# Optimization experiments

Hardware: AMD Instinct MI355X
Metric: run time of the kernel (lower is better)

## Reference

```python
import jax, jax.numpy as jnp
import numpy as np

V, C, T, H, HS, HID, L = 8000, 256, 256, 4, 64, 1024, 2
B = 2


def _ln(x, g, b, eps=1e-5):
    mu = jnp.mean(x, axis=-1, keepdims=True)
    var = jnp.var(x, axis=-1, keepdims=True)
    return (x - mu) * jax.lax.rsqrt(var + eps) * g + b


def setup_inputs() -> dict:
    key = jax.random.key(0)
    ks = iter(jax.random.split(key, 32))
    n = lambda shape: jax.random.normal(next(ks), shape, dtype=jnp.float32) * 0.02
    inp = {
        "idx": jax.random.randint(next(ks), (B, T), 0, V),
        "tok_emb": n((V, C)),
        # distance positional embedding params
        "pos_table": n((T, C)),
        "pos_w1": n((C, 2 * C)),
        "pos_w2": n((2 * C, 2 * C)),
        "pos_b2": n((2 * C,)),
        "pos_ln_g": jnp.ones((2 * C,), jnp.float32),
        "pos_ln_b": jnp.zeros((2 * C,), jnp.float32),
        # per-layer, per-head attention-MLP params (stacked over L, H)
        "att_w1": n((L, H, 2 * C, C)),
        "att_w2": n((L, H, C)),
        "att_b2": n((L, H)),
        "val_w": n((L, H, C, HS)),
        "proj_w": n((L, C, C)),
        "proj_b": n((L, C)),
        "ln2_g": jnp.ones((L, C), jnp.float32),
        "ln2_b": jnp.zeros((L, C), jnp.float32),
        "ff_w1": n((L, C, HID)),
        "ff_w2": n((L, HID, C)),
        "ff_b2": n((L, C)),
        "lnf_g": jnp.ones((C,), jnp.float32),
        "lnf_b": jnp.zeros((C,), jnp.float32),
        "head_w": n((C, V)),
        "head_b": n((V,)),
    }
    return inp


def reference(idx, tok_emb, pos_table, pos_w1, pos_w2, pos_b2, pos_ln_g, pos_ln_b,
              att_w1, att_w2, att_b2, val_w, proj_w, proj_b, ln2_g, ln2_b,
              ff_w1, ff_w2, ff_b2, lnf_g, lnf_b, head_w, head_b):
    b, t = idx.shape
    gelu = lambda x: jax.nn.gelu(x, approximate=False)

    # distance positional embedding: tril(i - j) indices into table
    ar = jnp.arange(t)
    dist = jnp.tril(ar[:, None] - ar[None, :])            # [t,t] in [0, t)
    pe = pos_table[dist]                                   # [t,t,C]
    pe = gelu(pe @ pos_w1) @ pos_w2 + pos_b2               # [t,t,2C]
    pe = _ln(pe, pos_ln_g, pos_ln_b)                       # [t,t,2C]

    mask = jnp.tril(jnp.ones((t, t), bool))                # causal
    scale = C ** (-0.5)

    x = tok_emb[idx]                                       # [b,t,C]
    for l in range(L):
        # pairwise concat(key, query) + pos emb, shared across heads
        kk = jnp.broadcast_to(x[:, None, :, :], (b, t, t, C))   # k[b,i,j]=x[b,j]
        qq = jnp.broadcast_to(x[:, :, None, :], (b, t, t, C))   # q[b,i,j]=x[b,i]
        a2 = jnp.concatenate([kk, qq], axis=-1) + pe[None]       # [b,t,t,2C]
        h1 = gelu(jnp.einsum('btsz,hzc->bhtsc', a2, att_w1[l]))  # [b,H,t,t,C]
        wei = jnp.einsum('bhtsc,hc->bhts', h1, att_w2[l]) + att_b2[l][None, :, None, None]
        wei = wei * scale
        wei = jnp.where(mask[None, None], wei, -jnp.inf)
        wei = jax.nn.softmax(wei, axis=-1)                       # [b,H,t,t]
        v = jnp.einsum('btc,hcd->bhtd', x, val_w[l])             # [b,H,t,HS]
        out = jnp.einsum('bhts,bhsd->bhtd', wei, v)              # [b,H,t,HS]
        out = out.transpose(0, 2, 1, 3).reshape(b, t, H * HS)    # concat heads
        x = x + out @ proj_w[l] + proj_b[l]
        h = _ln(x, ln2_g[l], ln2_b[l])
        x = x + gelu(h @ ff_w1[l]) @ ff_w2[l] + ff_b2[l]
    x = _ln(x, lnf_g, lnf_b)
    logits = x @ head_w + head_b                                 # [b,t,V]
    return logits
```

## Files before the change

### kernel.cpp

```cpp
#include <hip/hip_runtime.h>
#include <hip/hip_bf16.h>
#include <math.h>

constexpr int TDIM = 256;
constexpr int CDIM = 256;
constexpr int NH   = 4;
constexpr int DHS  = 64;
constexpr int FHID = 1024;
constexpr int NV   = 8000;
constexpr int NB   = 2;

typedef __attribute__((ext_vector_type(8))) short bf16x8;
typedef __attribute__((ext_vector_type(4))) float f32x4;
typedef __attribute__((ext_vector_type(2))) float f32x2;
typedef __attribute__((ext_vector_type(4))) unsigned int uint4v;

__device__ __forceinline__ float gelu_f(float x) {
    return 0.5f * x * (1.0f + erff(x * 0.70710678118654752440f));
}

__device__ __forceinline__ f32x2 gelu2p(f32x2 x) {
    constexpr float A = 0.7814073f, B = -0.1075621f, C = 0.00904825f, D = -0.000293447f;
    f32x2 xc;
    xc.x = fminf(fmaxf(x.x, -3.4f), 3.4f);
    xc.y = fminf(fmaxf(x.y, -3.4f), 3.4f);
    f32x2 u = xc * xc;
    f32x2 h = u * D + C;
    h = h * u + B;
    h = h * u + A;
    f32x2 g = xc * h;
    f32x2 t = x * 0.5f;
    return t * g + t;
}

__device__ __forceinline__ unsigned short f2bf(float f) {
    unsigned int u = __float_as_uint(f);
    unsigned int r = (u + 0x7FFF + ((u >> 16) & 1)) >> 16;
    return (unsigned short)r;
}

__global__ __launch_bounds__(256) void k_tcast_all(
    const float* __restrict__ head_w, const float* __restrict__ att_w1,
    const float* __restrict__ ff_w1, const float* __restrict__ ff_w2,
    const float* __restrict__ val_w, const float* __restrict__ proj_w,
    unsigned short* __restrict__ wT, unsigned short* __restrict__ W1r,
    unsigned short* __restrict__ Wff1, unsigned short* __restrict__ Wff2,
    unsigned short* __restrict__ Wv, unsigned short* __restrict__ Wproj)
{
    int q = blockIdx.x;
    const float* src; unsigned short* dst; int R, C, tx, ty;
    if (q < 2000)      { src = head_w; dst = wT; R = 256; C = 8000; tx = q % 250; ty = q / 250; }
    else if (q < 3024) { int u = q - 2000, s = u >> 7, v = u & 127;
        src = att_w1 + (size_t)s * 512 * 256; dst = W1r + (size_t)s * 512 * 256;
        R = 512; C = 256; tx = v & 7; ty = v >> 3; }
    else if (q < 3536) { int u = q - 3024, s = u >> 8, v = u & 255;
        src = ff_w1 + (size_t)s * 256 * 1024; dst = Wff1 + (size_t)s * 256 * 1024;
        R = 256; C = 1024; tx = v & 31; ty = v >> 5; }
    else if (q < 4048) { int u = q - 3536, s = u >> 8, v = u & 255;
        src = ff_w2 + (size_t)s * 1024 * 256; dst = Wff2 + (size_t)s * 1024 * 256;
        R = 1024; C = 256; tx = v & 7; ty = v >> 3; }
    else if (q < 4176) { int u = q - 4048, s = u >> 4, v = u & 15;
        src = val_w + (size_t)s * 256 * 64; dst = Wv + (size_t)s * 256 * 64;
        R = 256; C = 64; tx = v & 1; ty = v >> 1; }
    else { int u = q - 4176, s = u >> 6, v = u & 63;
        src = proj_w + (size_t)s * 256 * 256; dst = Wproj + (size_t)s * 256 * 256;
        R = 256; C = 256; tx = v & 7; ty = v >> 3; }
    __shared__ float tile[32][33];
    int c0 = tx * 32, r0 = ty * 32, t = threadIdx.x;
    #pragma unroll
    for (int e = 0; e < 4; ++e) {
        int lin = e * 256 + t; int rr = lin >> 5, cc = lin & 31;
        tile[rr][cc] = src[(size_t)(r0 + rr) * C + c0 + cc];
    }
    __syncthreads();
    #pragma unroll
    for (int e = 0; e < 4; ++e) {
        int lin = e * 256 + t; int cc = lin >> 5, rr = lin & 31;
        dst[(size_t)(c0 + cc) * R + r0 + rr] = f2bf(tile[rr][cc]);
    }
}

__global__ __launch_bounds__(512) void k_pre(
    const int* __restrict__ idx, const float* __restrict__ tok_emb,
    const float* __restrict__ pos_table, const float* __restrict__ pos_w1,
    const float* __restrict__ pos_w2, const float* __restrict__ pos_b2,
    const float* __restrict__ g, const float* __restrict__ bb,
    float* __restrict__ x, unsigned short* __restrict__ x_bf,
    unsigned short* __restrict__ ped_bf)
{
    int bid = blockIdx.x;
    int t = threadIdx.x;
    if (bid < 256) {
        int r = bid * 2 + (t >> 8);
        int c = t & 255;
        int tok = idx[r];
        float v = tok_emb[(size_t)tok * CDIM + c];
        x[r * CDIM + c] = v;
        x_bf[r * CDIM + c] = f2bf(v);
        return;
    }
    int d = bid - 256;
    __shared__ float xs[CDIM];
    __shared__ float hs[512];
    __shared__ float red[512];
    if (t < CDIM) xs[t] = pos_table[d * CDIM + t];
    __syncthreads();
    float acc = 0.f;
    for (int c = 0; c < CDIM; ++c) acc += xs[c] * pos_w1[(size_t)c * 512 + t];
    hs[t] = gelu_f(acc);
    __syncthreads();
    float acc2 = pos_b2[t];
    for (int z = 0; z < 512; ++z) acc2 += hs[z] * pos_w2[(size_t)z * 512 + t];
    red[t] = acc2; __syncthreads();
    for (int s = 256; s > 0; s >>= 1) { if (t < s) red[t] += red[t + s]; __syncthreads(); }
    float mean = red[0] * (1.f / 512.f); __syncthreads();
    float dv = acc2 - mean;
    red[t] = dv * dv; __syncthreads();
    for (int s = 256; s > 0; s >>= 1) { if (t < s) red[t] += red[t + s]; __syncthreads(); }
    float r = rsqrtf(red[0] * (1.f / 512.f) + 1e-5f);
    ped_bf[d * 512 + t] = f2bf(dv * r * g[t] + bb[t]);
}

__device__ __forceinline__ void gemm64_core(
    const unsigned short* __restrict__ A, int lda,
    const unsigned short* __restrict__ B, int ldb,
    int kLen, int t, f32x4 acc[2][2],
    unsigned short* __restrict__ A_lds, unsigned short* __restrict__ B_lds)
{
    int lane = t & 63;
    int w = t >> 6;
    int wm = (w >> 1) * 32, wn = (w & 1) * 32;
    int l15 = lane & 15;
    int lk = (lane >> 4) * 8;
    for (int kc = 0; kc < kLen; kc += 128) {
        #pragma unroll
        for (int it = 0; it < 4; ++it) {
            int chunk = it * 256 + t;
            int row = chunk >> 4;
            int c16 = chunk & 15;
            uint4v va = *(const uint4v*)(A + (size_t)row * lda + kc + c16 * 8);
            uint4v vb = *(const uint4v*)(B + (size_t)row * ldb + kc + c16 * 8);
            int lin = row * 256 + c16 * 16;
            int phys = lin ^ ((row & 7) << 4);
            *(uint4v*)((char*)A_lds + phys) = va;
            *(uint4v*)((char*)B_lds + phys) = vb;
        }
        __syncthreads();
        #pragma unroll
        for (int ks = 0; ks < 4; ++ks) {
            int kb = ks * 32 + lk;
            bf16x8 a[2], b[2];
            #pragma unroll
            for (int f = 0; f < 2; ++f) {
                int mrow = wm + f * 16 + l15;
                int lina = mrow * 256 + kb * 2;
                a[f] = *(const bf16x8*)((const char*)A_lds + (lina ^ ((mrow & 7) << 4)));
                int nrow = wn + f * 16 + l15;
                int linb = nrow * 256 + kb * 2;
                b[f] = *(const bf16x8*)((const char*)B_lds + (linb ^ ((nrow & 7) << 4)));
            }
            acc[0][0] = __builtin_amdgcn_mfma_f32_16x16x32_bf16(a[0], b[0], acc[0][0], 0, 0, 0);
            acc[0][1] = __builtin_amdgcn_mfma_f32_16x16x32_bf16(a[0], b[1], acc[0][1], 0, 0, 0);
            acc[1][0] = __builtin_amdgcn_mfma_f32_16x16x32_bf16(a[1], b[0], acc[1][0], 0, 0, 0);
            acc[1][1] = __builtin_amdgcn_mfma_f32_16x16x32_bf16(a[1], b[1], acc[1][1], 0, 0, 0);
        }
        __syncthreads();
    }
}

__global__ __launch_bounds__(256) void k_qkv(
    const unsigned short* __restrict__ x_bf,
    const unsigned short* __restrict__ ped_bf,
    const unsigned short* __restrict__ W1r,
    const unsigned short* __restrict__ Wv,
    float* __restrict__ PT, float* __restrict__ Qb, float* __restrict__ RT,
    unsigned short* __restrict__ vT_bf, int l)
{
    __shared__ unsigned short A_lds[64 * 128];
    __shared__ unsigned short B_lds[64 * 128];
    int t = threadIdx.x;
    int bid = blockIdx.x;
    int lane = t & 63, w = t >> 6;
    int wm = (w >> 1) * 32, wn = (w & 1) * 32;
    int l15 = lane & 15;
    f32x4 acc[2][2] = {};
    if (bid < 256) {
        int r0 = (bid & 7) * 64;
        int n0 = (bid >> 3) * 64;
        int h = n0 >> 9, isQ = (n0 >> 8) & 1;
        const unsigned short* Bp = W1r + (size_t)l * 1024 * 512
                                 + (size_t)(h * 256 + (n0 & 255)) * 512 + isQ * 256;
        gemm64_core(x_bf + (size_t)r0 * 256, 256, Bp, 512, 256, t, acc, A_lds, B_lds);
        #pragma unroll
        for (int fm = 0; fm < 2; ++fm)
        #pragma unroll
        for (int fn = 0; fn < 2; ++fn) {
            int col = n0 + wn + fn * 16 + l15;
            int c = col & 255;
            #pragma unroll
            for (int r = 0; r < 4; ++r) {
                int row = r0 + wm + fm * 16 + (lane >> 4) * 4 + r;
                int b = row >> 8, ij = row & 255;
                if (isQ) Qb[((b * TDIM + ij) * NH + h) * CDIM + c] = acc[fm][fn][r];
                else     PT[((size_t)(b * NH + h) * CDIM + c) * TDIM + ij] = acc[fm][fn][r];
            }
        }
    } else if (bid < 320) {
        int u = bid - 256;
        int r0 = (u & 3) * 64;
        int n0 = (u >> 2) * 64;
        const unsigned short* Bp = W1r + (size_t)l * 1024 * 512 + (size_t)n0 * 512;
        gemm64_core(ped_bf + (size_t)r0 * 512, 512, Bp, 512, 512, t, acc, A_lds, B_lds);
        #pragma unroll
        for (int fm = 0; fm < 2; ++fm)
        #pragma unroll
        for (int fn = 0; fn < 2; ++fn) {
            int col = n0 + wn + fn * 16 + l15;
            #pragma unroll
            for (int r = 0; r < 4; ++r) {
                int d = r0 + wm + fm * 16 + (lane >> 4) * 4 + r;
                RT[(size_t)col * TDIM + d] = acc[fm][fn][r];
            }
        }
    } else {
        int u = bid - 320;
        int r0 = (u & 7) * 64;
        int n0 = (u >> 3) * 64;
        int h = n0 >> 6;
        const unsigned short* Bp = Wv + ((size_t)l * NH + h) * DHS * CDIM;
        gemm64_core(x_bf + (size_t)r0 * 256, 256, Bp, 256, 256, t, acc, A_lds, B_lds);
        #pragma unroll
        for (int fm = 0; fm < 2; ++fm)
        #pragma unroll
        for (int fn = 0; fn < 2; ++fn) {
            int col = n0 + wn + fn * 16 + l15;
            int d = col & 63;
            #pragma unroll
            for (int r = 0; r < 4; ++r) {
                int row = r0 + wm + fm * 16 + (lane >> 4) * 4 + r;
                int b = row >> 8, j = row & 255;
                vT_bf[(((size_t)b * NH + h) * DHS + d) * TDIM + j] = f2bf(acc[fm][fn][r]);
            }
        }
    }
}

__global__ __launch_bounds__(1024, 8) void k_wei(
    const float* __restrict__ PT, const float* __restrict__ Qb,
    const float* __restrict__ RT, const float* __restrict__ att_w2,
    const float* __restrict__ att_b2, int l, unsigned short* __restrict__ wei_bf) {
    int bid = blockIdx.x;
    int bh = bid & 7;
    int b = bh >> 2, h = bh & 3;
    int i0 = (63 - (bid >> 3)) * 4;
    int t = threadIdx.x;
    int wid = t >> 6, lane = t & 63;
    int nlog = (i0 + 4 <= 64) ? 0 : (i0 + 4 <= 128) ? 1 : 2;
    int ns = 1 << nlog;
    int nchunks = 16 >> nlog;
    int c_len = 16 << nlog;
    int strip = wid & (ns - 1);
    int cchunk = wid >> nlog;
    int c0 = cchunk * c_len;
    int j = strip * 64 + lane;
    __shared__ float shQW[256][8];
    __shared__ float part[16][4][64];
    { int ii = t >> 8, c = t & 255;
      shQW[c][ii] = Qb[((b * TDIM + (i0 + ii)) * NH + h) * CDIM + c]; }
    if (t < 256) shQW[t][4] = att_w2[(l * NH + h) * CDIM + t];
    __syncthreads();
    f32x2 accA = {0.f, 0.f}, accB = {0.f, 0.f};
    int mm = max(i0 - j, -3);
    {
        const float* pk = PT + ((size_t)(b * NH + h) * CDIM + c0) * TDIM + j;
        const float* rk = RT + ((size_t)h * CDIM + c0) * TDIM + mm;
        #pragma unroll 4
        for (int k = 0; k < c_len; ++k) {
            float p = *pk;
            f32x4 r4; __builtin_memcpy(&r4, rk, 16);
            pk += TDIM; rk += TDIM;
            int c = c0 + k;
            f32x4 q4 = *(const f32x4*)(&shQW[c][0]);
            float w2v = shQW[c][4];
            f32x2 zA, zB;
            zA.x = p + q4.x + r4.x; zA.y = p + q4.y + r4.y;
            zB.x = p + q4.z + r4.z; zB.y = p + q4.w + r4.w;
            accA += gelu2p(zA) * w2v;
            accB += gelu2p(zB) * w2v;
        }
    }
    part[wid][0][lane] = accA.x; part[wid][1][lane] = accA.y;
    part[wid][2][lane] = accB.x; part[wid][3][lane] = accB.y;
    __syncthreads();
    if (t < 256) {
        int jj = t, sj = jj >> 6, l6 = jj & 63;
        float s0 = 0, s1 = 0, s2 = 0, s3 = 0;
        for (int cc = 0; cc < nchunks; ++cc) {
            int w = ((cc << nlog) + sj) & 15;
            s0 += part[w][0][l6]; s1 += part[w][1][l6];
            s2 += part[w][2][l6]; s3 += part[w][3][l6];
        }
        shQW[jj][0] = s0; shQW[jj][1] = s1; shQW[jj][2] = s2; shQW[jj][3] = s3;
    }
    __syncthreads();
    if (t < 256) {
        float b2 = att_b2[l * NH + h];
        int l6 = t & 63, w = t >> 6;
        int i = i0 + w;
        float lv[4];
        #pragma unroll
        for (int s = 0; s < 4; ++s) {
            int jj = l6 + s * 64;
            lv[s] = (jj <= i) ? (shQW[jj][w] + b2) * 0.0625f : -1e30f;
        }
        float mx = fmaxf(fmaxf(lv[0], lv[1]), fmaxf(lv[2], lv[3]));
        #pragma unroll
        for (int off = 32; off; off >>= 1) mx = fmaxf(mx, __shfl_xor(mx, off));
        float es[4], sum = 0.f;
        #pragma unroll
        for (int s = 0; s < 4; ++s) { es[s] = exp2f((lv[s] - mx) * 1.4426950409f); sum += es[s]; }
        #pragma unroll
        for (int off = 32; off; off >>= 1) sum += __shfl_xor(sum, off);
        float inv = 1.0f / sum;
        unsigned short* wrow = wei_bf + (((size_t)bh * TDIM) + i) * TDIM;
        #pragma unroll
        for (int s = 0; s < 4; ++s) wrow[l6 + s * 64] = f2bf(es[s] * inv);
    }
}

__global__ __launch_bounds__(256) void k_av_gemm(
    const unsigned short* __restrict__ wei_bf,
    const unsigned short* __restrict__ vT_bf,
    unsigned short* __restrict__ attn_bf)
{
    __shared__ unsigned short A_lds[64 * 128];
    __shared__ unsigned short B_lds[64 * 128];
    int t = threadIdx.x;
    int bid = blockIdx.x;
    int bh = bid >> 2;
    int r0 = (bid & 3) * 64;
    int b = bh >> 2, h = bh & 3;
    f32x4 acc[2][2] = {};
    gemm64_core(wei_bf + (size_t)bh * 65536 + (size_t)r0 * 256, 256,
                vT_bf + (size_t)bh * 16384, 256, 256, t, acc, A_lds, B_lds);
    int lane = t & 63, w = t >> 6;
    int wm = (w >> 1) * 32, wn = (w & 1) * 32;
    int l15 = lane & 15;
    #pragma unroll
    for (int fm = 0; fm < 2; ++fm)
    #pragma unroll
    for (int fn = 0; fn < 2; ++fn) {
        int d = wn + fn * 16 + l15;
        #pragma unroll
        for (int r = 0; r < 4; ++r) {
            int i = r0 + wm + fm * 16 + (lane >> 4) * 4 + r;
            attn_bf[((size_t)(b * TDIM + i)) * CDIM + h * DHS + d] = f2bf(acc[fm][fn][r]);
        }
    }
}

__global__ __launch_bounds__(256) void k_proj_gemm(
    const unsigned short* __restrict__ attn_bf,
    const unsigned short* __restrict__ Wproj,
    const float* __restrict__ proj_b,
    float* __restrict__ pbuf, int l)
{
    __shared__ unsigned short A_lds[64 * 128];
    __shared__ unsigned short B_lds[64 * 128];
    int t = threadIdx.x;
    int r0 = (blockIdx.x & 7) * 64;
    int n0 = (blockIdx.x >> 3) * 64;
    f32x4 acc[2][2] = {};
    gemm64_core(attn_bf + (size_t)r0 * 256, 256,
                Wproj + (size_t)l * 65536 + (size_t)n0 * 256, 256, 256, t, acc, A_lds, B_lds);
    int lane = t & 63, w = t >> 6;
    int wm = (w >> 1) * 32, wn = (w & 1) * 32;
    int l15 = lane & 15;
    #pragma unroll
    for (int fm = 0; fm < 2; ++fm)
    #pragma unroll
    for (int fn = 0; fn < 2; ++fn) {
        int col = n0 + wn + fn * 16 + l15;
        float bb = proj_b[l * CDIM + col];
        #pragma unroll
        for (int r = 0; r < 4; ++r) {
            int row = r0 + wm + fm * 16 + (lane >> 4) * 4 + r;
            pbuf[(size_t)row * CDIM + col] = acc[fm][fn][r] + bb;
        }
    }
}

__global__ void k_resln(const float* __restrict__ pbuf, float* __restrict__ x,
                        const float* __restrict__ lg, const float* __restrict__ lb,
                        unsigned short* __restrict__ hbuf_bf) {
    int bi = blockIdx.x;
    int t = threadIdx.x;
    __shared__ float red[CDIM];
    float val = x[bi * CDIM + t] + pbuf[bi * CDIM + t];
    x[bi * CDIM + t] = val;
    red[t] = val; __syncthreads();
    for (int s = 128; s > 0; s >>= 1) { if (t < s) red[t] += red[t + s]; __syncthreads(); }
    float mean = red[0] * (1.f / 256.f); __syncthreads();
    float dv = val - mean;
    red[t] = dv * dv; __syncthreads();
    for (int s = 128; s > 0; s >>= 1) { if (t < s) red[t] += red[t + s]; __syncthreads(); }
    float r = rsqrtf(red[0] * (1.f / 256.f) + 1e-5f);
    hbuf_bf[bi * CDIM + t] = f2bf(dv * r * lg[t] + lb[t]);
}

__global__ __launch_bounds__(256) void k_ff1_gemm(
    const unsigned short* __restrict__ hbuf_bf,
    const unsigned short* __restrict__ Wff1,
    unsigned short* __restrict__ fbuf_bf, int l)
{
    __shared__ unsigned short A_lds[64 * 128];
    __shared__ unsigned short B_lds[64 * 128];
    int t = threadIdx.x;
    int r0 = blockIdx.x * 64;
    int n0 = blockIdx.y * 64;
    const unsigned short* Bp = Wff1 + (size_t)l * 1024 * 256 + (size_t)n0 * 256;
    f32x4 acc[2][2] = {};
    gemm64_core(hbuf_bf + (size_t)r0 * 256, 256, Bp, 256, 256, t, acc, A_lds, B_lds);
    int lane = t & 63, w = t >> 6;
    int wm = (w >> 1) * 32, wn = (w & 1) * 32;
    int l15 = lane & 15;
    #pragma unroll
    for (int fm = 0; fm < 2; ++fm)
    #pragma unroll
    for (int fn = 0; fn < 2; ++fn) {
        int col = n0 + wn + fn * 16 + l15;
        #pragma unroll
        for (int r = 0; r < 4; ++r) {
            int row = r0 + wm + fm * 16 + (lane >> 4) * 4 + r;
            fbuf_bf[(size_t)row * FHID + col] = f2bf(gelu_f(acc[fm][fn][r]));
        }
    }
}

__global__ __launch_bounds__(256) void k_ff2_gemm(
    const unsigned short* __restrict__ fbuf_bf,
    const unsigned short* __restrict__ Wff2,
    const float* __restrict__ ff_b2,
    float* __restrict__ x, unsigned short* __restrict__ x_bf, int l)
{
    __shared__ unsigned short A_lds[64 * 128];
    __shared__ unsigned short B_lds[64 * 128];
    int t = threadIdx.x;
    int r0 = blockIdx.x * 64;
    int n0 = blockIdx.y * 64;
    const unsigned short* Bp = Wff2 + (size_t)l * 256 * 1024 + (size_t)n0 * 1024;
    f32x4 acc[2][2] = {};
    gemm64_core(fbuf_bf + (size_t)r0 * 1024, 1024, Bp, 1024, 1024, t, acc, A_lds, B_lds);
    int lane = t & 63, w = t >> 6;
    int wm = (w >> 1) * 32, wn = (w & 1) * 32;
    int l15 = lane & 15;
    #pragma unroll
    for (int fm = 0; fm < 2; ++fm)
    #pragma unroll
    for (int fn = 0; fn < 2; ++fn) {
        int col = n0 + wn + fn * 16 + l15;
        float bb = ff_b2[l * CDIM + col];
        #pragma unroll
        for (int r = 0; r < 4; ++r) {
            int row = r0 + wm + fm * 16 + (lane >> 4) * 4 + r;
            float v = x[(size_t)row * CDIM + col] + acc[fm][fn][r] + bb;
            x[(size_t)row * CDIM + col] = v;
            x_bf[(size_t)row * CDIM + col] = f2bf(v);
        }
    }
}

__global__ void k_lnf_bf16(const float* __restrict__ x, const float* __restrict__ g,
                           const float* __restrict__ bb, unsigned short* __restrict__ out) {
    int bi = blockIdx.x;
    int t = threadIdx.x;
    __shared__ float red[CDIM];
    float val = x[bi * CDIM + t];
    red[t] = val; __syncthreads();
    for (int s = 128; s > 0; s >>= 1) { if (t < s) red[t] += red[t + s]; __syncthreads(); }
    float mean = red[0] * (1.f / 256.f); __syncthreads();
    float dv = val - mean;
    red[t] = dv * dv; __syncthreads();
    for (int s = 128; s > 0; s >>= 1) { if (t < s) red[t] += red[t + s]; __syncthreads(); }
    float r = rsqrtf(red[0] * (1.f / 256.f) + 1e-5f);
    out[bi * CDIM + t] = f2bf(dv * r * g[t] + bb[t]);
}

__global__ __launch_bounds__(256) void k_head_mfma(
    const unsigned short* __restrict__ xf_bf,
    const unsigned short* __restrict__ wT,
    const float* __restrict__ head_b,
    float* __restrict__ out)
{
    __shared__ unsigned short A_lds[64 * 128];
    __shared__ unsigned short B_lds[64 * 128];
    int t = threadIdx.x;
    int r0 = blockIdx.x * 64;
    int n0 = blockIdx.y * 64;
    f32x4 acc[2][2] = {};
    gemm64_core(xf_bf + (size_t)r0 * 256, 256, wT + (size_t)n0 * 256, 256, 256,
                t, acc, A_lds, B_lds);
    int lane = t & 63, w = t >> 6;
    int wm = (w >> 1) * 32, wn = (w & 1) * 32;
    int l15 = lane & 15;
    #pragma unroll
    for (int fm = 0; fm < 2; ++fm)
    #pragma unroll
    for (int fn = 0; fn < 2; ++fn) {
        int col = n0 + wn + fn * 16 + l15;
        float hb = head_b[col];
        #pragma unroll
        for (int r = 0; r < 4; ++r) {
            int row = r0 + wm + fm * 16 + (lane >> 4) * 4 + r;
            out[(size_t)row * NV + col] = acc[fm][fn][r] + hb;
        }
    }
}

extern "C" void kernel_launch(void* const* d_in, const int* in_sizes, int n_in,
                              void* d_out, int out_size, void* d_ws, size_t ws_size,
                              hipStream_t stream) {
    const int*   idx       = (const int*)  d_in[0];
    const float* tok_emb   = (const float*)d_in[1];
    const float* pos_table = (const float*)d_in[2];
    const float* pos_w1    = (const float*)d_in[3];
    const float* pos_w2    = (const float*)d_in[4];
    const float* pos_b2    = (const float*)d_in[5];
    const float* pos_ln_g  = (const float*)d_in[6];
    const float* pos_ln_b  = (const float*)d_in[7];
    const float* att_w1    = (const float*)d_in[8];
    const float* att_w2    = (const float*)d_in[9];
    const float* att_b2    = (const float*)d_in[10];
    const float* val_w     = (const float*)d_in[11];
    const float* proj_w    = (const float*)d_in[12];
    const float* proj_b    = (const float*)d_in[13];
    const float* ln2_g     = (const float*)d_in[14];
    const float* ln2_b     = (const float*)d_in[15];
    const float* ff_w1     = (const float*)d_in[16];
    const float* ff_w2     = (const float*)d_in[17];
    const float* ff_b2     = (const float*)d_in[18];
    const float* lnf_g     = (const float*)d_in[19];
    const float* lnf_b     = (const float*)d_in[20];
    const float* head_w    = (const float*)d_in[21];
    const float* head_b    = (const float*)d_in[22];
    float* out = (float*)d_out;

    float* ws = (float*)d_ws;
    float* x    = ws;  ws += NB * TDIM * CDIM;
    float* PT   = ws;  ws += NB * NH * CDIM * TDIM;
    float* Qb   = ws;  ws += NB * TDIM * NH * CDIM;
    ws += 16;
    float* RT   = ws;  ws += NH * CDIM * TDIM;
    float* pbuf = PT;
    unsigned short* x_bf    = (unsigned short*)ws; ws += NB * TDIM * CDIM / 2;
    unsigned short* ped_bf  = (unsigned short*)ws; ws += TDIM * 2 * CDIM / 2;
    unsigned short* hbuf_bf = (unsigned short*)ws; ws += NB * TDIM * CDIM / 2;
    unsigned short* xf_bf   = (unsigned short*)ws; ws += NB * TDIM * CDIM / 2;
    unsigned short* wei_bf  = (unsigned short*)ws; ws += NB * NH * TDIM * TDIM / 2;
    unsigned short* vT_bf   = (unsigned short*)ws; ws += NB * NH * DHS * TDIM / 2;
    unsigned short* attn_bf = (unsigned short*)ws; ws += NB * TDIM * CDIM / 2;
    unsigned short* wT      = (unsigned short*)ws; ws += NV * CDIM / 2;
    unsigned short* W1r     = (unsigned short*)ws; ws += 2 * 1024 * 512 / 2;
    unsigned short* Wff1    = (unsigned short*)ws; ws += 2 * 1024 * 256 / 2;
    unsigned short* Wff2    = (unsigned short*)ws; ws += 2 * 256 * 1024 / 2;
    unsigned short* Wv      = (unsigned short*)ws; ws += 2 * NH * DHS * CDIM / 2;
    unsigned short* Wproj   = (unsigned short*)ws; ws += 2 * CDIM * CDIM / 2;
    unsigned short* fbuf_bf = wei_bf;

    k_tcast_all<<<4304, 256, 0, stream>>>(head_w, att_w1, ff_w1, ff_w2, val_w, proj_w,
                                          wT, W1r, Wff1, Wff2, Wv, Wproj);
    k_pre<<<512, 512, 0, stream>>>(idx, tok_emb, pos_table, pos_w1, pos_w2, pos_b2,
                                   pos_ln_g, pos_ln_b, x, x_bf, ped_bf);

    for (int l = 0; l < 2; ++l) {
        k_qkv<<<352, 256, 0, stream>>>(x_bf, ped_bf, W1r, Wv, PT, Qb, RT, vT_bf, l);
        k_wei<<<NB * NH * TDIM / 4, 1024, 0, stream>>>(PT, Qb, RT, att_w2, att_b2, l, wei_bf);
        k_av_gemm<<<32, 256, 0, stream>>>(wei_bf, vT_bf, attn_bf);
        k_proj_gemm<<<32, 256, 0, stream>>>(attn_bf, Wproj, proj_b, pbuf, l);
        k_resln<<<NB * TDIM, 256, 0, stream>>>(pbuf, x, ln2_g + l * CDIM, ln2_b + l * CDIM, hbuf_bf);
        k_ff1_gemm<<<dim3(8, 16), 256, 0, stream>>>(hbuf_bf, Wff1, fbuf_bf, l);
        k_ff2_gemm<<<dim3(8, 4), 256, 0, stream>>>(fbuf_bf, Wff2, ff_b2, x, x_bf, l);
    }

    k_lnf_bf16<<<NB * TDIM, 256, 0, stream>>>(x, lnf_g, lnf_b, xf_bf);
    k_head_mfma<<<dim3(8, 125), 256, 0, stream>>>(xf_bf, wT, head_b, out);
}
```

Measured before the change: 282.7 us.

## Fold value and output projections into one weight; retile head GEMM to 128x128

Each head's value weight is multiplied by its slice of the output projection in the setup kernel, giving a combined 256x256 bf16 weight per layer and head. Each head's value-times-projection is then computed directly in the QKV kernel, so one fused kernel computes the attention-weighted sum plus the projection by accumulating over heads. This drops one kernel launch and the intermediate attention buffer, but raises the FLOPs in the QKV kernel and makes each of the 32 fused blocks loop over four heads. Separately, the vocabulary head GEMM moves from 64x64 to 128x128 tiles with 4x4 MFMA fragments per wave and bounds-checked output columns. That cuts the block count and improves reuse, at the cost of fewer blocks than compute units and padded reads past the vocabulary edge.

```diff
diff --git a/kernel.cpp b/kernel.cpp
--- a/kernel.cpp
+++ b/kernel.cpp
@@ -45,9 +45,44 @@
     const float* __restrict__ val_w, const float* __restrict__ proj_w,
     unsigned short* __restrict__ wT, unsigned short* __restrict__ W1r,
     unsigned short* __restrict__ Wff1, unsigned short* __restrict__ Wff2,
-    unsigned short* __restrict__ Wv, unsigned short* __restrict__ Wproj)
+    unsigned short* __restrict__ WcomboT)
 {
     int q = blockIdx.x;
+    int t = threadIdx.x;
+    if (q >= 4048) {
+        int u = q - 4048;
+        int lh = u >> 4;
+        int c0 = (u & 15) * 16;
+        __shared__ float val16[16][64];
+        __shared__ unsigned short tmp[256][16];
+        #pragma unroll
+        for (int e = 0; e < 4; ++e) {
+            int lin = e * 256 + t;
+            int cc = lin >> 6, d = lin & 63;
+            val16[cc][d] = val_w[((size_t)lh * 256 + c0 + cc) * 64 + d];
+        }
+        __syncthreads();
+        float acc[16];
+        #pragma unroll
+        for (int cc = 0; cc < 16; ++cc) acc[cc] = 0.f;
+        const float* pw = proj_w + ((size_t)(lh >> 2) * 256 + (lh & 3) * 64) * 256 + t;
+        for (int d = 0; d < 64; ++d) {
+            float p = pw[(size_t)d * 256];
+            #pragma unroll
+            for (int cc = 0; cc < 16; ++cc) acc[cc] = fmaf(val16[cc][d], p, acc[cc]);
+        }
+        #pragma unroll
+        for (int cc = 0; cc < 16; ++cc) tmp[t][cc] = f2bf(acc[cc]);
+        __syncthreads();
+        unsigned short* dst = WcomboT + (size_t)lh * 65536;
+        #pragma unroll
+        for (int p = 0; p < 16; ++p) {
+            int idx = p * 256 + t;
+            int n = idx >> 4, cc = idx & 15;
+            dst[(size_t)n * 256 + c0 + cc] = tmp[n][cc];
+        }
+        return;
+    }
     const float* src; unsigned short* dst; int R, C, tx, ty;
     if (q < 2000)      { src = head_w; dst = wT; R = 256; C = 8000; tx = q % 250; ty = q / 250; }
     else if (q < 3024) { int u = q - 2000, s = u >> 7, v = u & 127;
@@ -56,17 +91,11 @@
     else if (q < 3536) { int u = q - 3024, s = u >> 8, v = u & 255;
         src = ff_w1 + (size_t)s * 256 * 1024; dst = Wff1 + (size_t)s * 256 * 1024;
         R = 256; C = 1024; tx = v & 31; ty = v >> 5; }
-    else if (q < 4048) { int u = q - 3536, s = u >> 8, v = u & 255;
+    else { int u = q - 3536, s = u >> 8, v = u & 255;
         src = ff_w2 + (size_t)s * 1024 * 256; dst = Wff2 + (size_t)s * 1024 * 256;
         R = 1024; C = 256; tx = v & 7; ty = v >> 3; }
-    else if (q < 4176) { int u = q - 4048, s = u >> 4, v = u & 15;
-        src = val_w + (size_t)s * 256 * 64; dst = Wv + (size_t)s * 256 * 64;
-        R = 256; C = 64; tx = v & 1; ty = v >> 1; }
-    else { int u = q - 4176, s = u >> 6, v = u & 63;
-        src = proj_w + (size_t)s * 256 * 256; dst = Wproj + (size_t)s * 256 * 256;
-        R = 256; C = 256; tx = v & 7; ty = v >> 3; }
     __shared__ float tile[32][33];
-    int c0 = tx * 32, r0 = ty * 32, t = threadIdx.x;
+    int c0 = tx * 32, r0 = ty * 32;
     #pragma unroll
     for (int e = 0; e < 4; ++e) {
         int lin = e * 256 + t; int rr = lin >> 5, cc = lin & 31;
@@ -172,9 +201,9 @@
     const unsigned short* __restrict__ x_bf,
     const unsigned short* __restrict__ ped_bf,
     const unsigned short* __restrict__ W1r,
-    const unsigned short* __restrict__ Wv,
+    const unsigned short* __restrict__ WcomboT,
     float* __restrict__ PT, float* __restrict__ Qb, float* __restrict__ RT,
-    unsigned short* __restrict__ vT_bf, int l)
+    unsigned short* __restrict__ uT_bf, int l)
 {
     __shared__ unsigned short A_lds[64 * 128];
     __shared__ unsigned short B_lds[64 * 128];
@@ -224,22 +253,22 @@
         }
     } else {
         int u = bid - 320;
-        int r0 = (u & 7) * 64;
-        int n0 = (u >> 3) * 64;
-        int h = n0 >> 6;
-        const unsigned short* Bp = Wv + ((size_t)l * NH + h) * DHS * CDIM;
-        gemm64_core(x_bf + (size_t)r0 * 256, 256, Bp, 256, 256, t, acc, A_lds, B_lds);
+        int bh = u >> 4;
+        int tile = u & 15;
+        int r0 = (tile & 3) * 64;
+        int n0 = (tile >> 2) * 64;
+        int b = bh >> 2, h = bh & 3;
+        const unsigned short* Bp = WcomboT + (size_t)(l * 4 + h) * 65536 + (size_t)n0 * 256;
+        gemm64_core(x_bf + (size_t)(b * 256 + r0) * 256, 256, Bp, 256, 256, t, acc, A_lds, B_lds);
         #pragma unroll
         for (int fm = 0; fm < 2; ++fm)
         #pragma unroll
         for (int fn = 0; fn < 2; ++fn) {
             int col = n0 + wn + fn * 16 + l15;
-            int d = col & 63;
             #pragma unroll
             for (int r = 0; r < 4; ++r) {
                 int row = r0 + wm + fm * 16 + (lane >> 4) * 4 + r;
-                int b = row >> 8, j = row & 255;
-                vT_bf[(((size_t)b * NH + h) * DHS + d) * TDIM + j] = f2bf(acc[fm][fn][r]);
+                uT_bf[((size_t)bh * 256 + col) * 256 + row] = f2bf(acc[fm][fn][r]);
             }
         }
     }
@@ -328,51 +357,25 @@
     }
 }
 
-__global__ __launch_bounds__(256) void k_av_gemm(
+__global__ __launch_bounds__(256) void k_avp_gemm(
     const unsigned short* __restrict__ wei_bf,
-    const unsigned short* __restrict__ vT_bf,
-    unsigned short* __restrict__ attn_bf)
+    const unsigned short* __restrict__ uT_bf,
+    const float* __restrict__ proj_b,
+    float* __restrict__ pbuf, int l)
 {
     __shared__ unsigned short A_lds[64 * 128];
     __shared__ unsigned short B_lds[64 * 128];
     int t = threadIdx.x;
-    int bid = blockIdx.x;
-    int bh = bid >> 2;
-    int r0 = (bid & 3) * 64;
-    int b = bh >> 2, h = bh & 3;
-    f32x4 acc[2][2] = {};
-    gemm64_core(wei_bf + (size_t)bh * 65536 + (size_t)r0 * 256, 256,
-                vT_bf + (size_t)bh * 16384, 256, 256, t, acc, A_lds, B_lds);
-    int lane = t & 63, w = t >> 6;
-    int wm = (w >> 1) * 32, wn = (w & 1) * 32;
-    int l15 = lane & 15;
-    #pragma unroll
-    for (int fm = 0; fm < 2; ++fm)
-    #pragma unroll
-    for (int fn = 0; fn < 2; ++fn) {
-        int d = wn + fn * 16 + l15;
-        #pragma unroll
-        for (int r = 0; r < 4; ++r) {
-            int i = r0 + wm + fm * 16 + (lane >> 4) * 4 + r;
-            attn_bf[((size_t)(b * TDIM + i)) * CDIM + h * DHS + d] = f2bf(acc[fm][fn][r]);
-        }
-    }
-}
-
-__global__ __launch_bounds__(256) void k_proj_gemm(
-    const unsigned short* __restrict__ attn_bf,
-    const unsigned short* __restrict__ Wproj,
-    const float* __restrict__ proj_b,
-    float* __restrict__ pbuf, int l)
-{
-    __shared__ unsigned short A_lds[64 * 128];
-    __shared__ unsigned short B_lds[64 * 128];
-    int t = threadIdx.x;
     int r0 = (blockIdx.x & 7) * 64;
     int n0 = (blockIdx.x >> 3) * 64;
+    int b = r0 >> 8, ir = r0 & 255;
     f32x4 acc[2][2] = {};
-    gemm64_core(attn_bf + (size_t)r0 * 256, 256,
-                Wproj + (size_t)l * 65536 + (size_t)n0 * 256, 256, 256, t, acc, A_lds, B_lds);
+    #pragma unroll
+    for (int h = 0; h < 4; ++h) {
+        gemm64_core(wei_bf + (size_t)(b * 4 + h) * 65536 + (size_t)ir * 256, 256,
+                    uT_bf + (size_t)(b * 4 + h) * 65536 + (size_t)n0 * 256, 256,
+                    256, t, acc, A_lds, B_lds);
+    }
     int lane = t & 63, w = t >> 6;
     int wm = (w >> 1) * 32, wn = (w & 1) * 32;
     int l15 = lane & 15;
@@ -492,27 +495,63 @@
     const float* __restrict__ head_b,
     float* __restrict__ out)
 {
-    __shared__ unsigned short A_lds[64 * 128];
-    __shared__ unsigned short B_lds[64 * 128];
-    int t = threadIdx.x;
-    int r0 = blockIdx.x * 64;
-    int n0 = blockIdx.y * 64;
-    f32x4 acc[2][2] = {};
-    gemm64_core(xf_bf + (size_t)r0 * 256, 256, wT + (size_t)n0 * 256, 256, 256,
-                t, acc, A_lds, B_lds);
+    __shared__ unsigned short A_lds[128 * 128];
+    __shared__ unsigned short B_lds[128 * 128];
+    int t = threadIdx.x;
+    int r0 = blockIdx.x * 128;
+    int n0 = blockIdx.y * 128;
     int lane = t & 63, w = t >> 6;
-    int wm = (w >> 1) * 32, wn = (w & 1) * 32;
+    int wr = (w >> 1) * 64, wc = (w & 1) * 64;
     int l15 = lane & 15;
-    #pragma unroll
-    for (int fm = 0; fm < 2; ++fm)
-    #pragma unroll
-    for (int fn = 0; fn < 2; ++fn) {
-        int col = n0 + wn + fn * 16 + l15;
-        float hb = head_b[col];
-        #pragma unroll
-        for (int r = 0; r < 4; ++r) {
-            int row = r0 + wm + fm * 16 + (lane >> 4) * 4 + r;
-            out[(size_t)row * NV + col] = acc[fm][fn][r] + hb;
+    int lk = (lane >> 4) * 8;
+    f32x4 acc[4][4] = {};
+    for (int kc = 0; kc < 256; kc += 128) {
+        #pragma unroll
+        for (int it = 0; it < 8; ++it) {
+            int chunk = it * 256 + t;
+            int row = chunk >> 4;
+            int c16 = chunk & 15;
+            uint4v va = *(const uint4v*)(xf_bf + (size_t)(r0 + row) * 256 + kc + c16 * 8);
+            uint4v vb = *(const uint4v*)(wT + (size_t)(n0 + row) * 256 + kc + c16 * 8);
+            int lin = row * 256 + c16 * 16;
+            int phys = lin ^ ((row & 7) << 4);
+            *(uint4v*)((char*)A_lds + phys) = va;
+            *(uint4v*)((char*)B_lds + phys) = vb;
+        }
+        __syncthreads();
+        #pragma unroll
+        for (int ks = 0; ks < 4; ++ks) {
+            int kb = ks * 32 + lk;
+            bf16x8 a[4], b[4];
+            #pragma unroll
+            for (int f = 0; f < 4; ++f) {
+                int mrow = wr + f * 16 + l15;
+                int lina = mrow * 256 + kb * 2;
+                a[f] = *(const bf16x8*)((const char*)A_lds + (lina ^ ((mrow & 7) << 4)));
+                int nrow = wc + f * 16 + l15;
+                int linb = nrow * 256 + kb * 2;
+                b[f] = *(const bf16x8*)((const char*)B_lds + (linb ^ ((nrow & 7) << 4)));
+            }
+            #pragma unroll
+            for (int fm = 0; fm < 4; ++fm)
+            #pragma unroll
+            for (int fn = 0; fn < 4; ++fn)
+                acc[fm][fn] = __builtin_amdgcn_mfma_f32_16x16x32_bf16(a[fm], b[fn], acc[fm][fn], 0, 0, 0);
+        }
+        __syncthreads();
+    }
+    #pragma unroll
+    for (int fm = 0; fm < 4; ++fm)
+    #pragma unroll
+    for (int fn = 0; fn < 4; ++fn) {
+        int col = n0 + wc + fn * 16 + l15;
+        if (col < NV) {
+            float hb = head_b[col];
+            #pragma unroll
+            for (int r = 0; r < 4; ++r) {
+                int row = r0 + wr + fm * 16 + (lane >> 4) * 4 + r;
+                out[(size_t)row * NV + col] = acc[fm][fn][r] + hb;
+            }
         }
     }
 }
@@ -557,31 +596,28 @@
     unsigned short* hbuf_bf = (unsigned short*)ws; ws += NB * TDIM * CDIM / 2;
     unsigned short* xf_bf   = (unsigned short*)ws; ws += NB * TDIM * CDIM / 2;
     unsigned short* wei_bf  = (unsigned short*)ws; ws += NB * NH * TDIM * TDIM / 2;
-    unsigned short* vT_bf   = (unsigned short*)ws; ws += NB * NH * DHS * TDIM / 2;
-    unsigned short* attn_bf = (unsigned short*)ws; ws += NB * TDIM * CDIM / 2;
+    unsigned short* uT_bf   = (unsigned short*)ws; ws += NB * NH * TDIM * TDIM / 2;
     unsigned short* wT      = (unsigned short*)ws; ws += NV * CDIM / 2;
     unsigned short* W1r     = (unsigned short*)ws; ws += 2 * 1024 * 512 / 2;
     unsigned short* Wff1    = (unsigned short*)ws; ws += 2 * 1024 * 256 / 2;
     unsigned short* Wff2    = (unsigned short*)ws; ws += 2 * 256 * 1024 / 2;
-    unsigned short* Wv      = (unsigned short*)ws; ws += 2 * NH * DHS * CDIM / 2;
-    unsigned short* Wproj   = (unsigned short*)ws; ws += 2 * CDIM * CDIM / 2;
+    unsigned short* WcomboT = (unsigned short*)ws; ws += 2 * NH * CDIM * CDIM / 2;
     unsigned short* fbuf_bf = wei_bf;
 
-    k_tcast_all<<<4304, 256, 0, stream>>>(head_w, att_w1, ff_w1, ff_w2, val_w, proj_w,
-                                          wT, W1r, Wff1, Wff2, Wv, Wproj);
+    k_tcast_all<<<4176, 256, 0, stream>>>(head_w, att_w1, ff_w1, ff_w2, val_w, proj_w,
+                                          wT, W1r, Wff1, Wff2, WcomboT);
     k_pre<<<512, 512, 0, stream>>>(idx, tok_emb, pos_table, pos_w1, pos_w2, pos_b2,
                                    pos_ln_g, pos_ln_b, x, x_bf, ped_bf);
 
     for (int l = 0; l < 2; ++l) {
-        k_qkv<<<352, 256, 0, stream>>>(x_bf, ped_bf, W1r, Wv, PT, Qb, RT, vT_bf, l);
+        k_qkv<<<448, 256, 0, stream>>>(x_bf, ped_bf, W1r, WcomboT, PT, Qb, RT, uT_bf, l);
         k_wei<<<NB * NH * TDIM / 4, 1024, 0, stream>>>(PT, Qb, RT, att_w2, att_b2, l, wei_bf);
-        k_av_gemm<<<32, 256, 0, stream>>>(wei_bf, vT_bf, attn_bf);
-        k_proj_gemm<<<32, 256, 0, stream>>>(attn_bf, Wproj, proj_b, pbuf, l);
+        k_avp_gemm<<<32, 256, 0, stream>>>(wei_bf, uT_bf, proj_b, pbuf, l);
         k_resln<<<NB * TDIM, 256, 0, stream>>>(pbuf, x, ln2_g + l * CDIM, ln2_b + l * CDIM, hbuf_bf);
         k_ff1_gemm<<<dim3(8, 16), 256, 0, stream>>>(hbuf_bf, Wff1, fbuf_bf, l);
         k_ff2_gemm<<<dim3(8, 4), 256, 0, stream>>>(fbuf_bf, Wff2, ff_b2, x, x_bf, l);
     }
 
     k_lnf_bf16<<<NB * TDIM, 256, 0, stream>>>(x, lnf_g, lnf_b, xf_bf);
-    k_head_mfma<<<dim3(8, 125), 256, 0, stream>>>(xf_bf, wT, head_b, out);
-}
+    k_head_mfma<<<dim3(4, 63), 256, 0, stream>>>(xf_bf, wT, head_b, out);
+}
```

Result: slower. 293.0 us (+3.6%).
